# Performance work log

Hardware: AMD Instinct MI355X
Metric: run time of the kernel (lower is better)

Reference implementation:

```python
import jax, jax.numpy as jnp
import numpy as np

N = 50000      # nodes
E = 500000     # edges
IN = 256       # input feature dim
HID = 64       # hidden (per-head) dim, layer 1
H1 = 4         # heads, layer 1
NC = 64        # num_classes (layer 2 out, 1 head)
ED = 32        # edge_dim
T = 8          # num_etypes
SLOPE = 0.2    # leakyrelu negative slope


def setup_inputs() -> dict:
    key = jax.random.key(0)
    ks = jax.random.split(key, 20)
    p = lambda k, shape: (jax.random.normal(k, shape, jnp.float32) * 0.05)
    return {
        "h": jax.random.normal(ks[0], (N, IN), jnp.float32),
        "row": jax.random.randint(ks[1], (E,), 0, N, jnp.int32),   # src
        "col": jax.random.randint(ks[2], (E,), 0, N, jnp.int32),   # dst
        "etype": jax.random.randint(ks[3], (E,), 0, T, jnp.int32),
        # layer 1 (4 heads, no residual, elu activation)
        "edge_emb1": p(ks[4], (T, ED)),
        "W1": p(ks[5], (IN, HID * H1)),
        "Wr1": p(ks[6], (T, ED, ED * H1)),      # TypedLinear per-etype weight
        "a_l1": p(ks[7], (H1, HID)),
        "a_r1": p(ks[8], (H1, HID)),
        "a_e1": p(ks[9], (H1, ED)),
        # layer 2 (1 head, residual Linear, no activation)
        "edge_emb2": p(ks[10], (T, ED)),
        "W2": p(ks[11], (HID * H1, NC)),
        "Wr2": p(ks[12], (T, ED, ED)),
        "a_l2": p(ks[13], (1, NC)),
        "a_r2": p(ks[14], (1, NC)),
        "a_e2": p(ks[15], (1, ED)),
        "res_W2": p(ks[16], (HID * H1, NC)),
        "res_b2": p(ks[17], (NC,)),
    }


def _simple_hgn_conv(h, row, col, etype, edge_emb, W, Wr, a_l, a_r, a_e,
                     res_W, res_b, apply_act):
    """One SimpleHGNConv layer. h:[N,in], returns [N, out_dim*H] (D-major, H-minor
    layout, matching emb.permute(0,2,1).view in the torch code)."""
    H, D = a_l.shape            # num_heads, out_dim
    n = h.shape[0]
    emb = (h @ W).reshape(n, H, D)                     # [N,H,D]
    emb = jnp.where(jnp.isnan(emb), 0.0, emb)
    # TypedLinear: edge_emb[etype] @ Wr[etype]; only T distinct rows -> per-type GEMM
    ee = jnp.einsum('te,teo->to', edge_emb, Wr).reshape(T, H, ED)  # [T,H,ED]
    h_l = jnp.einsum('nhd,hd->nh', emb, a_l)[row]      # [E,H]
    h_r = jnp.einsum('nhd,hd->nh', emb, a_r)[col]      # [E,H]
    h_e = jnp.einsum('thd,hd->th', ee, a_e)[etype]     # [E,H]
    att = jax.nn.leaky_relu(h_l + h_r + h_e, SLOPE)    # [E,H]
    # edge_softmax: normalize over incoming edges of each destination node (col)
    seg_max = jax.ops.segment_max(att, col, num_segments=n)   # [N,H]
    att = jnp.exp(att - seg_max[col])
    seg_sum = jax.ops.segment_sum(att, col, num_segments=n)   # [N,H]
    alpha = att / seg_sum[col]                          # [E,H]
    # u_mul_e + sum aggregation
    msg = emb[row] * alpha[:, :, None]                  # [E,H,D]
    out = jax.ops.segment_sum(msg, col, num_segments=n) # [N,H,D]
    out = out.transpose(0, 2, 1).reshape(n, D * H)      # D-major layout
    if res_W is not None:
        out = out + h @ res_W + res_b
    if apply_act:
        out = jax.nn.elu(out)
    return out


def reference(h, row, col, etype,
              edge_emb1, W1, Wr1, a_l1, a_r1, a_e1,
              edge_emb2, W2, Wr2, a_l2, a_r2, a_e2, res_W2, res_b2):
    h1 = _simple_hgn_conv(h, row, col, etype, edge_emb1, W1, Wr1,
                          a_l1, a_r1, a_e1, None, None, True)
    h2 = _simple_hgn_conv(h1, row, col, etype, edge_emb2, W2, Wr2,
                          a_l2, a_r2, a_e2, res_W2, res_b2, False)
    # split by node type (first half type 'l', second half type 'v')
    return (h2[: N // 2], h2[N // 2 :])
```

## Files before the change

### kernel.cpp

```cpp
#include <hip/hip_runtime.h>
#include <hip/hip_bf16.h>

typedef __bf16 bf16x8 __attribute__((ext_vector_type(8)));
typedef float f32x4 __attribute__((ext_vector_type(4)));

#define IN_DIM 256
#define NT 8

__device__ __forceinline__ float b2f(unsigned short u) {
  union { unsigned int i; float f; } x; x.i = ((unsigned int)u) << 16; return x.f;
}
__device__ __forceinline__ float lo2f(unsigned int w) {
  union { unsigned int i; float f; } x; x.i = w << 16; return x.f;
}
__device__ __forceinline__ float hi2f(unsigned int w) {
  union { unsigned int i; float f; } x; x.i = w & 0xFFFF0000u; return x.f;
}
__device__ __forceinline__ unsigned short f2b(float f) {
  union { float f; unsigned int i; } u; u.f = f;
  unsigned int r = u.i + 0x7FFF + ((u.i >> 16) & 1);
  return (unsigned short)(r >> 16);
}
__device__ __forceinline__ float lrelu(float x) { return x >= 0.f ? x : 0.2f * x; }
__device__ __forceinline__ float ldf(const void* p, size_t i, int isf32) {
  return isf32 ? ((const float*)p)[i] : b2f(((const unsigned short*)p)[i]);
}

__global__ void detect_kernel(const unsigned int* __restrict__ hw, int* __restrict__ flag) {
  int tid = threadIdx.x;
  int bad = 0;
  for (int i = 0; i < 4; i++) {
    unsigned int w = hw[tid * 4 + i];
    unsigned int e = (w & 0x7FFFu) >> 7;
    if (e >= 0xC0u) bad++;
  }
#pragma unroll
  for (int off = 32; off; off >>= 1) bad += __shfl_xor(bad, off);
  if (tid == 0) *flag = (bad > 8) ? 1 : 0;
}

__global__ void prep_all_kernel(const void* __restrict__ W1, const void* __restrict__ W2,
                                const void* __restrict__ rW2,
                                const void* __restrict__ al1, const void* __restrict__ ar1,
                                const void* __restrict__ al2, const void* __restrict__ ar2,
                                const void* __restrict__ ee1, const void* __restrict__ Wr1,
                                const void* __restrict__ ae1,
                                const void* __restrict__ ee2, const void* __restrict__ Wr2,
                                const void* __restrict__ ae2,
                                unsigned short* __restrict__ W1t,
                                unsigned short* __restrict__ W2t,
                                float* __restrict__ a2l, float* __restrict__ a2r,
                                float* __restrict__ he1, float* __restrict__ he2,
                                float* __restrict__ alD, float* __restrict__ arD,
                                const int* __restrict__ dflag) {
  int isf32 = *dflag;
  int b = blockIdx.x, tid = threadIdx.x;
  if (b < 384) {
    int j = b, k = tid;
    if (j < 256) {
      int src = (j & 3) * 64 + (j >> 2);
      W1t[j * 256 + k] = f2b(ldf(W1, (size_t)k * 256 + src, isf32));
    } else {
      int o = j - 256;
      float v = (o < 64) ? ldf(W2, (size_t)k * 64 + o, isf32)
                         : ldf(rW2, (size_t)k * 64 + (o - 64), isf32);
      W2t[o * 256 + k] = f2b(v);
    }
  } else if (b < 448) {
    int k = (b - 384) * 4 + (tid >> 6), d = tid & 63;
    float w2 = ldf(W2, (size_t)k * 64 + d, isf32);
    float l2 = w2 * ldf(al2, d, isf32);
    float r2 = w2 * ldf(ar2, d, isf32);
#pragma unroll
    for (int off = 32; off; off >>= 1) { l2 += __shfl_xor(l2, off); r2 += __shfl_xor(r2, off); }
    if (d == 0) { a2l[k] = l2; a2r[k] = r2; }
  } else {
    int bid = b - 448;
    int t = tid >> 5, d = tid & 31;
    if (bid < 4) {
      int h = bid;
      float s = 0.f;
#pragma unroll
      for (int e = 0; e < 32; e++)
        s += ldf(ee1, t * 32 + e, isf32) * ldf(Wr1, (size_t)(t * 32 + e) * 128 + h * 32 + d, isf32);
      float v = s * ldf(ae1, h * 32 + d, isf32);
#pragma unroll
      for (int off = 16; off; off >>= 1) v += __shfl_xor(v, off);
      if (d == 0) he1[t * 4 + h] = v;
    } else if (bid == 4) {
      float s = 0.f;
#pragma unroll
      for (int e = 0; e < 32; e++)
        s += ldf(ee2, t * 32 + e, isf32) * ldf(Wr2, (size_t)(t * 32 + e) * 32 + d, isf32);
      float v = s * ldf(ae2, d, isf32);
#pragma unroll
      for (int off = 16; off; off >>= 1) v += __shfl_xor(v, off);
      if (d == 0) he2[t] = v;
    } else {
      int j = tid;
      alD[j] = ldf(al1, (j & 3) * 64 + (j >> 2), isf32);
      arD[j] = ldf(ar1, (j & 3) * 64 + (j >> 2), isf32);
    }
  }
}

__global__ __launch_bounds__(256, 2) void gemm1_fused(
    const void* __restrict__ A, int M,
    const unsigned short* __restrict__ Bt,
    unsigned short* __restrict__ emb1,
    const float* __restrict__ alD, const float* __restrict__ arD,
    float* __restrict__ hl1, float* __restrict__ hr1,
    const int* __restrict__ dflag) {
  __shared__ unsigned short As[64 * 64];
  __shared__ unsigned short Bs[256 * 64];
  __shared__ float lsum[4][64][4];
  __shared__ float rsum[4][64][4];
  int isf32 = *dflag;
  const int tid = threadIdx.x;
  const int m0 = blockIdx.x * 64;
  const int wv = tid >> 6, lane = tid & 63;
  const int q = lane >> 4, m = lane & 15;
  const int jp = wv * 64;
  f32x4 acc[4][4] = {};
  for (int kc = 0; kc < 256; kc += 64) {
    {
      int row = tid >> 2, qt = tid & 3;
      int gr = m0 + row;
      unsigned short tmp[16];
      if (gr < M) {
        if (isf32) {
          const float* ap = (const float*)A + (size_t)gr * 256 + kc + qt * 16;
          float4 v0 = *(const float4*)ap;
          float4 v1 = *(const float4*)(ap + 4);
          float4 v2 = *(const float4*)(ap + 8);
          float4 v3 = *(const float4*)(ap + 12);
          tmp[0]=f2b(v0.x); tmp[1]=f2b(v0.y); tmp[2]=f2b(v0.z); tmp[3]=f2b(v0.w);
          tmp[4]=f2b(v1.x); tmp[5]=f2b(v1.y); tmp[6]=f2b(v1.z); tmp[7]=f2b(v1.w);
          tmp[8]=f2b(v2.x); tmp[9]=f2b(v2.y); tmp[10]=f2b(v2.z); tmp[11]=f2b(v2.w);
          tmp[12]=f2b(v3.x); tmp[13]=f2b(v3.y); tmp[14]=f2b(v3.z); tmp[15]=f2b(v3.w);
        } else {
          const unsigned short* ap = (const unsigned short*)A + (size_t)gr * 256 + kc + qt * 16;
          *(int4*)tmp = *(const int4*)ap;
          *(int4*)(tmp + 8) = *(const int4*)(ap + 8);
        }
      } else {
        for (int x = 0; x < 16; x++) tmp[x] = 0;
      }
      int g0 = (qt * 2) ^ (row & 7);
      int g1 = (qt * 2 + 1) ^ (row & 7);
      *(int4*)(As + row * 64 + g0 * 8) = *(int4*)tmp;
      *(int4*)(As + row * 64 + g1 * 8) = *(int4*)(tmp + 8);
    }
    {
#pragma unroll
      for (int i = 0; i < 8; i++) {
        int id = tid + i * 256;
        int row = id >> 3, gg = id & 7;
        int4 v = *(const int4*)(Bt + (size_t)row * 256 + kc + gg * 8);
        int pg = gg ^ (row & 7);
        *(int4*)(Bs + row * 64 + pg * 8) = v;
      }
    }
    __syncthreads();
#pragma unroll
    for (int ks = 0; ks < 2; ks++) {
      int gk = ks * 4 + q;
      bf16x8 afr[4];
#pragma unroll
      for (int cm = 0; cm < 4; cm++) {
        int row = cm * 16 + m;
        afr[cm] = *(const bf16x8*)(As + row * 64 + (gk ^ (row & 7)) * 8);
      }
#pragma unroll
      for (int cj = 0; cj < 4; cj++) {
        int jr = jp + cj * 16 + m;
        bf16x8 b = *(const bf16x8*)(Bs + jr * 64 + (gk ^ (jr & 7)) * 8);
#pragma unroll
        for (int cm = 0; cm < 4; cm++)
          acc[cm][cj] = __builtin_amdgcn_mfma_f32_16x16x32_bf16(afr[cm], b, acc[cm][cj], 0, 0, 0);
      }
    }
    __syncthreads();
  }
  float al[4], ar[4];
#pragma unroll
  for (int cj = 0; cj < 4; cj++) {
    al[cj] = alD[jp + cj * 16 + m];
    ar[cj] = arD[jp + cj * 16 + m];
  }
#pragma unroll
  for (int cm = 0; cm < 4; cm++) {
#pragma unroll
    for (int r = 0; r < 4; r++) {
      int lrow = cm * 16 + q * 4 + r;
      int gm = m0 + lrow;
      float lp = 0.f, rp = 0.f;
#pragma unroll
      for (int cj = 0; cj < 4; cj++) {
        float v = acc[cm][cj][r];
        if (gm < M) emb1[(size_t)gm * 256 + jp + cj * 16 + m] = f2b(v);
        lp += v * al[cj]; rp += v * ar[cj];
      }
      lp += __shfl_xor(lp, 4); lp += __shfl_xor(lp, 8);
      rp += __shfl_xor(rp, 4); rp += __shfl_xor(rp, 8);
      if (m < 4) { lsum[wv][lrow][m] = lp; rsum[wv][lrow][m] = rp; }
    }
  }
  __syncthreads();
  {
    int row = tid >> 2, h = tid & 3;
    int gm = m0 + row;
    if (gm < M) {
      float l = lsum[0][row][h] + lsum[1][row][h] + lsum[2][row][h] + lsum[3][row][h];
      float r = rsum[0][row][h] + rsum[1][row][h] + rsum[2][row][h] + rsum[3][row][h];
      hl1[(size_t)gm * 4 + h] = l;
      hr1[(size_t)gm * 4 + h] = r;
    }
  }
}

__global__ __launch_bounds__(256, 2) void gemm2_fused(
    const unsigned short* __restrict__ A, int M,
    const unsigned short* __restrict__ Bt,
    unsigned short* __restrict__ emb2, unsigned short* __restrict__ res,
    const void* __restrict__ bias, const int* __restrict__ dflag) {
  __shared__ unsigned short As[64 * 64];
  __shared__ unsigned short Bs[128 * 64];
  int isf32 = *dflag;
  const int tid = threadIdx.x;
  const int m0 = blockIdx.x * 64;
  const int wv = tid >> 6, lane = tid & 63;
  const int q = lane >> 4, m = lane & 15;
  const int jp = (wv & 1) * 64;
  const int mh = (wv >> 1) * 32;
  f32x4 acc[2][4] = {};
  for (int kc = 0; kc < 256; kc += 64) {
    {
      int row = tid >> 2, qt = tid & 3;
      int gr = m0 + row;
      unsigned short tmp[16];
      if (gr < M) {
        const unsigned short* ap = A + (size_t)gr * 256 + kc + qt * 16;
        *(int4*)tmp = *(const int4*)ap;
        *(int4*)(tmp + 8) = *(const int4*)(ap + 8);
      } else {
        for (int x = 0; x < 16; x++) tmp[x] = 0;
      }
      int g0 = (qt * 2) ^ (row & 7);
      int g1 = (qt * 2 + 1) ^ (row & 7);
      *(int4*)(As + row * 64 + g0 * 8) = *(int4*)tmp;
      *(int4*)(As + row * 64 + g1 * 8) = *(int4*)(tmp + 8);
    }
    {
#pragma unroll
      for (int i = 0; i < 4; i++) {
        int id = tid + i * 256;
        int row = id >> 3, gg = id & 7;
        int4 v = *(const int4*)(Bt + (size_t)row * 256 + kc + gg * 8);
        int pg = gg ^ (row & 7);
        *(int4*)(Bs + row * 64 + pg * 8) = v;
      }
    }
    __syncthreads();
#pragma unroll
    for (int ks = 0; ks < 2; ks++) {
      int gk = ks * 4 + q;
      bf16x8 afr[2];
#pragma unroll
      for (int cm = 0; cm < 2; cm++) {
        int row = mh + cm * 16 + m;
        afr[cm] = *(const bf16x8*)(As + row * 64 + (gk ^ (row & 7)) * 8);
      }
#pragma unroll
      for (int cj = 0; cj < 4; cj++) {
        int jr = jp + cj * 16 + m;
        bf16x8 b = *(const bf16x8*)(Bs + jr * 64 + (gk ^ (jr & 7)) * 8);
#pragma unroll
        for (int cm = 0; cm < 2; cm++)
          acc[cm][cj] = __builtin_amdgcn_mfma_f32_16x16x32_bf16(afr[cm], b, acc[cm][cj], 0, 0, 0);
      }
    }
    __syncthreads();
  }
  float bv[4];
#pragma unroll
  for (int cj = 0; cj < 4; cj++)
    bv[cj] = (jp == 64) ? ldf(bias, cj * 16 + m, isf32) : 0.f;
#pragma unroll
  for (int cm = 0; cm < 2; cm++) {
#pragma unroll
    for (int r = 0; r < 4; r++) {
      int gm = m0 + mh + cm * 16 + q * 4 + r;
      if (gm < M) {
#pragma unroll
        for (int cj = 0; cj < 4; cj++) {
          float v = acc[cm][cj][r];
          int gj = cj * 16 + m;
          if (jp == 0) emb2[(size_t)gm * 64 + gj] = f2b(v);
          else res[(size_t)gm * 64 + gj] = f2b(v + bv[cj]);
        }
      }
    }
  }
}

__global__ void count_kernel(const int* __restrict__ col, int* __restrict__ cnt,
                             int E_, int N_) {
  int e = blockIdx.x * 256 + threadIdx.x;
  if (e >= E_) return;
  int c = col[e];
  if ((unsigned)c < (unsigned)N_) atomicAdd(&cnt[c], 1);
}

__global__ void scan1_kernel(const int* __restrict__ cnt, int* __restrict__ ptrb,
                             int* __restrict__ bsum, int n) {
  __shared__ int wsum[4];
  int tid = threadIdx.x, lane = tid & 63, wid = tid >> 6;
  int i = blockIdx.x * 256 + tid;
  int v = (i < n) ? cnt[i] : 0;
  int x = v;
#pragma unroll
  for (int off = 1; off < 64; off <<= 1) {
    int y = __shfl_up(x, off);
    if (lane >= off) x += y;
  }
  if (lane == 63) wsum[wid] = x;
  __syncthreads();
  int woff = 0;
#pragma unroll
  for (int k = 0; k < 4; k++) woff += (k < wid) ? wsum[k] : 0;
  if (i < n) ptrb[i] = x - v + woff;
  if (tid == 255) bsum[blockIdx.x] = woff + x;
}

__global__ void scan2_kernel(int* __restrict__ bsum, int* __restrict__ ptrb,
                             int nb, int n) {
  __shared__ int wsum[4];
  int tid = threadIdx.x, lane = tid & 63, wid = tid >> 6;
  int v = (tid < nb) ? bsum[tid] : 0;
  int x = v;
#pragma unroll
  for (int off = 1; off < 64; off <<= 1) {
    int y = __shfl_up(x, off);
    if (lane >= off) x += y;
  }
  if (lane == 63) wsum[wid] = x;
  __syncthreads();
  int woff = 0;
#pragma unroll
  for (int k = 0; k < 4; k++) woff += (k < wid) ? wsum[k] : 0;
  if (tid < nb) bsum[tid] = x - v + woff;
  if (tid == 255) ptrb[n] = woff + x;
}

__global__ void scan3_kernel(int* __restrict__ ptrb, const int* __restrict__ bsum, int n) {
  int i = blockIdx.x * 256 + threadIdx.x;
  if (i < n) ptrb[i] += bsum[blockIdx.x];
}

__global__ void fill_kernel(const int* __restrict__ col, const int* __restrict__ row,
                            const int* __restrict__ ety, const int* __restrict__ ptrb,
                            int* __restrict__ cnt, int* __restrict__ srcc, int E_, int N_) {
  int e = blockIdx.x * 256 + threadIdx.x;
  if (e >= E_) return;
  int c = col[e];
  if ((unsigned)c >= (unsigned)N_) return;
  int pos = atomicSub(&cnt[c], 1) - 1;
  long long slot = (long long)ptrb[c] + pos;
  if (slot >= 0 && slot < E_) {
    int sr = row[e], t = ety[e];
    srcc[slot] = ((unsigned)sr < (unsigned)N_ && (unsigned)t < (unsigned)NT)
                     ? (sr | (t << 20)) : -1;
  }
}

__global__ __launch_bounds__(256) void agg1_kernel(
    const int* __restrict__ ptrb, const int* __restrict__ srcc,
    const float* __restrict__ hl1, const float* __restrict__ hr1,
    const float* __restrict__ he1,
    const unsigned short* __restrict__ emb1, unsigned short* __restrict__ h1,
    const float* __restrict__ a2l, const float* __restrict__ a2r,
    float* __restrict__ hl2, float* __restrict__ hr2,
    int N_, int E_) {
  __shared__ float4 wds[4][64];
  __shared__ int sds[4][64];
  const int tid = threadIdx.x;
  const int wv = tid >> 6, lane = tid & 63;
  const int g = lane >> 4, ln = lane & 15;
  const int node = blockIdx.x * 16 + wv * 4 + g;
  const bool nv = node < N_;
  int p0 = 0, p1 = 0;
  if (nv) {
    p0 = ptrb[node]; p1 = ptrb[node + 1];
    p0 = max(0, min(p0, E_)); p1 = max(p0, min(p1, E_));
  }
  float4 hrv = {0.f, 0.f, 0.f, 0.f};
  if (nv) hrv = *(const float4*)(hr1 + 4 * (size_t)node);
  float s0 = 0.f, s1 = 0.f, s2 = 0.f, s3 = 0.f;
  float acc[16];
#pragma unroll
  for (int k = 0; k < 16; k++) acc[k] = 0.f;
  const unsigned short* erow = emb1 + ln * 16;
  for (int pb = p0;; pb += 16) {
    if (!__any(pb < p1)) break;
    int mc = (pb < p1) ? min(p1 - pb, 16) : 0;
    float4 w = {0.f, 0.f, 0.f, 0.f};
    int src = 0;
    if (ln < mc) {
      int spk = srcc[pb + ln];
      if (spk >= 0) {
        int sr = spk & 0xFFFFF, t = spk >> 20;
        float4 a = *(const float4*)(hl1 + 4 * (size_t)sr);
        float4 ge = *(const float4*)(he1 + 4 * (size_t)t);
        w.x = __expf(lrelu(a.x + hrv.x + ge.x));
        w.y = __expf(lrelu(a.y + hrv.y + ge.y));
        w.z = __expf(lrelu(a.z + hrv.z + ge.z));
        w.w = __expf(lrelu(a.w + hrv.w + ge.w));
        src = sr;
      }
    }
    s0 += w.x; s1 += w.y; s2 += w.z; s3 += w.w;
    wds[wv][lane] = w;
    sds[wv][lane] = src;
    for (int j = 0; j < mc; j += 2) {
      bool v1 = (j + 1) < mc;
      float4 u0 = wds[wv][g * 16 + j];
      int r0 = sds[wv][g * 16 + j];
      const unsigned short* e0 = erow + (size_t)r0 * 256;
      int4 ra = *(const int4*)e0;
      int4 rb = *(const int4*)(e0 + 8);
      float4 u1; int4 rc, rd;
      if (v1) {
        u1 = wds[wv][g * 16 + j + 1];
        int r1 = sds[wv][g * 16 + j + 1];
        const unsigned short* e1 = erow + (size_t)r1 * 256;
        rc = *(const int4*)e1;
        rd = *(const int4*)(e1 + 8);
      }
      acc[0]  += u0.x * lo2f(ra.x); acc[1]  += u0.y * hi2f(ra.x);
      acc[2]  += u0.z * lo2f(ra.y); acc[3]  += u0.w * hi2f(ra.y);
      acc[4]  += u0.x * lo2f(ra.z); acc[5]  += u0.y * hi2f(ra.z);
      acc[6]  += u0.z * lo2f(ra.w); acc[7]  += u0.w * hi2f(ra.w);
      acc[8]  += u0.x * lo2f(rb.x); acc[9]  += u0.y * hi2f(rb.x);
      acc[10] += u0.z * lo2f(rb.y); acc[11] += u0.w * hi2f(rb.y);
      acc[12] += u0.x * lo2f(rb.z); acc[13] += u0.y * hi2f(rb.z);
      acc[14] += u0.z * lo2f(rb.w); acc[15] += u0.w * hi2f(rb.w);
      if (v1) {
        acc[0]  += u1.x * lo2f(rc.x); acc[1]  += u1.y * hi2f(rc.x);
        acc[2]  += u1.z * lo2f(rc.y); acc[3]  += u1.w * hi2f(rc.y);
        acc[4]  += u1.x * lo2f(rc.z); acc[5]  += u1.y * hi2f(rc.z);
        acc[6]  += u1.z * lo2f(rc.w); acc[7]  += u1.w * hi2f(rc.w);
        acc[8]  += u1.x * lo2f(rd.x); acc[9]  += u1.y * hi2f(rd.x);
        acc[10] += u1.z * lo2f(rd.y); acc[11] += u1.w * hi2f(rd.y);
        acc[12] += u1.x * lo2f(rd.z); acc[13] += u1.y * hi2f(rd.z);
        acc[14] += u1.z * lo2f(rd.w); acc[15] += u1.w * hi2f(rd.w);
      }
    }
  }
#pragma unroll
  for (int off = 1; off < 16; off <<= 1) {
    s0 += __shfl_xor(s0, off); s1 += __shfl_xor(s1, off);
    s2 += __shfl_xor(s2, off); s3 += __shfl_xor(s3, off);
  }
  float invs[4];
  invs[0] = s0 > 0.f ? 1.f / s0 : 0.f;
  invs[1] = s1 > 0.f ? 1.f / s1 : 0.f;
  invs[2] = s2 > 0.f ? 1.f / s2 : 0.f;
  invs[3] = s3 > 0.f ? 1.f / s3 : 0.f;
  float alv[16], arv[16];
#pragma unroll
  for (int q2 = 0; q2 < 4; q2++) {
    float4 t1 = *(const float4*)(a2l + ln * 16 + q2 * 4);
    float4 t2 = *(const float4*)(a2r + ln * 16 + q2 * 4);
    alv[q2 * 4 + 0] = t1.x; alv[q2 * 4 + 1] = t1.y;
    alv[q2 * 4 + 2] = t1.z; alv[q2 * 4 + 3] = t1.w;
    arv[q2 * 4 + 0] = t2.x; arv[q2 * 4 + 1] = t2.y;
    arv[q2 * 4 + 2] = t2.z; arv[q2 * 4 + 3] = t2.w;
  }
  float lp = 0.f, rp = 0.f;
  unsigned int ow[8];
#pragma unroll
  for (int k = 0; k < 16; k++) {
    float r = acc[k] * invs[k & 3];
    r = r > 0.f ? r : __expf(r) - 1.f;
    unsigned int bb = f2b(r);
    if ((k & 1) == 0) ow[k >> 1] = bb; else ow[k >> 1] |= bb << 16;
    lp += r * alv[k];
    rp += r * arv[k];
  }
  if (nv) {
    int4 va; va.x = ow[0]; va.y = ow[1]; va.z = ow[2]; va.w = ow[3];
    int4 vb; vb.x = ow[4]; vb.y = ow[5]; vb.z = ow[6]; vb.w = ow[7];
    *(int4*)(h1 + (size_t)node * 256 + ln * 16) = va;
    *(int4*)(h1 + (size_t)node * 256 + ln * 16 + 8) = vb;
  }
#pragma unroll
  for (int off = 1; off < 16; off <<= 1) {
    lp += __shfl_xor(lp, off); rp += __shfl_xor(rp, off);
  }
  if (nv && ln == 0) { hl2[node] = lp; hr2[node] = rp; }
}

__global__ __launch_bounds__(256) void agg2_kernel(
    const int* __restrict__ ptrb, const int* __restrict__ srcc,
    const float* __restrict__ hl2, const float* __restrict__ hr2,
    const float* __restrict__ he2,
    const unsigned short* __restrict__ emb2, const unsigned short* __restrict__ res,
    void* __restrict__ out, int N_, int E_, const int* __restrict__ dflag) {
  __shared__ int2 wsd[4][64];
  const int isf32 = *dflag;
  const int tid = threadIdx.x;
  const int wv = tid >> 6, lane = tid & 63;
  const int g = lane >> 4, ln = lane & 15;
  const int node = blockIdx.x * 16 + wv * 4 + g;
  const bool nv = node < N_;
  int p0 = 0, p1 = 0;
  if (nv) {
    p0 = ptrb[node]; p1 = ptrb[node + 1];
    p0 = max(0, min(p0, E_)); p1 = max(p0, min(p1, E_));
  }
  float hrv = nv ? hr2[node] : 0.f;
  float s = 0.f;
  float acc[4] = {0.f, 0.f, 0.f, 0.f};
  const unsigned short* erow = emb2 + ln * 4;
  for (int pb = p0;; pb += 16) {
    if (!__any(pb < p1)) break;
    int mc = (pb < p1) ? min(p1 - pb, 16) : 0;
    float w = 0.f; int src = 0;
    if (ln < mc) {
      int spk = srcc[pb + ln];
      if (spk >= 0) {
        int sr = spk & 0xFFFFF, t = spk >> 20;
        w = __expf(lrelu(hl2[sr] + hrv + he2[t]));
        src = sr;
      }
    }
    s += w;
    int2 pk; pk.x = __float_as_int(w); pk.y = src;
    wsd[wv][lane] = pk;
    for (int j = 0; j < mc; j += 2) {
      bool v1 = (j + 1) < mc;
      int2 w0 = wsd[wv][g * 16 + j];
      float u0 = __int_as_float(w0.x);
      int2 ra = *(const int2*)(erow + (size_t)w0.y * 64);
      float u1 = 0.f; int2 rc;
      if (v1) {
        int2 w1 = wsd[wv][g * 16 + j + 1];
        u1 = __int_as_float(w1.x);
        rc = *(const int2*)(erow + (size_t)w1.y * 64);
      }
      acc[0] += u0 * lo2f(ra.x); acc[1] += u0 * hi2f(ra.x);
      acc[2] += u0 * lo2f(ra.y); acc[3] += u0 * hi2f(ra.y);
      if (v1) {
        acc[0] += u1 * lo2f(rc.x); acc[1] += u1 * hi2f(rc.x);
        acc[2] += u1 * lo2f(rc.y); acc[3] += u1 * hi2f(rc.y);
      }
    }
  }
#pragma unroll
  for (int off = 1; off < 16; off <<= 1) s += __shfl_xor(s, off);
  float inv = s > 0.f ? 1.f / s : 0.f;
  if (nv) {
    ushort4 rv = *(const ushort4*)(res + (size_t)node * 64 + ln * 4);
    float o0 = acc[0] * inv + b2f(rv.x);
    float o1 = acc[1] * inv + b2f(rv.y);
    float o2 = acc[2] * inv + b2f(rv.z);
    float o3 = acc[3] * inv + b2f(rv.w);
    size_t oi = (size_t)node * 64 + ln * 4;
    if (isf32) {
      float4 ov = {o0, o1, o2, o3};
      *(float4*)((float*)out + oi) = ov;
    } else {
      ushort4 ov; ov.x = f2b(o0); ov.y = f2b(o1); ov.z = f2b(o2); ov.w = f2b(o3);
      *(ushort4*)((unsigned short*)out + oi) = ov;
    }
  }
}

extern "C" void kernel_launch(void* const* d_in, const int* in_sizes, int n_in,
                              void* d_out, int out_size, void* d_ws, size_t ws_size,
                              hipStream_t stream) {
  const int N = in_sizes[0] / IN_DIM;
  const int E = in_sizes[1];

  const void* h   = d_in[0];
  const int* row  = (const int*)d_in[1];
  const int* col  = (const int*)d_in[2];
  const int* ety  = (const int*)d_in[3];
  const void* ee1 = d_in[4];
  const void* W1  = d_in[5];
  const void* Wr1 = d_in[6];
  const void* al1 = d_in[7];
  const void* ar1 = d_in[8];
  const void* ae1 = d_in[9];
  const void* ee2 = d_in[10];
  const void* W2  = d_in[11];
  const void* Wr2 = d_in[12];
  const void* al2 = d_in[13];
  const void* ar2 = d_in[14];
  const void* ae2 = d_in[15];
  const void* rW2 = d_in[16];
  const void* rb2 = d_in[17];

  char* p = (char*)d_ws;
  auto take = [&](size_t b) { char* q = p; p += (b + 255) & ~(size_t)255; return q; };
  unsigned short* h1   = (unsigned short*)take((size_t)N * 256 * 2);
  unsigned short* emb1 = (unsigned short*)take((size_t)N * 256 * 2);
  int* srcc = (int*)take((size_t)E * 4);
  int* ptrb = (int*)take((size_t)(N + 1) * 4);
  int* cnt  = (int*)take((size_t)N * 4);
  int* bsum = (int*)take(1024);
  float* hl1 = (float*)take((size_t)N * 4 * 4);
  float* hr1 = (float*)take((size_t)N * 4 * 4);
  float* hl2 = (float*)take((size_t)N * 4);
  float* hr2 = (float*)take((size_t)N * 4);
  unsigned short* W1t = (unsigned short*)take(256 * 256 * 2);
  unsigned short* W2t = (unsigned short*)take(128 * 256 * 2);
  float* a2l = (float*)take(256 * 4);
  float* a2r = (float*)take(256 * 4);
  float* alD = (float*)take(256 * 4);
  float* arD = (float*)take(256 * 4);
  float* he1 = (float*)take(NT * 4 * 4);
  float* he2 = (float*)take(NT * 4);
  int* dflag = (int*)take(256);
  unsigned short* emb2 = emb1;
  unsigned short* res  = emb1 + (size_t)N * 64;

  const size_t need = (size_t)(p - (char*)d_ws);
  if (need > ws_size) {
    hipMemsetAsync(d_out, 0, (size_t)out_size * 2, stream);
    return;
  }

  const int EB = (E + 255) / 256;
  const int MB = (N + 63) / 64;
  const int SB = (N + 255) / 256;
  const int AB = (N + 15) / 16;

  detect_kernel<<<1, 64, 0, stream>>>((const unsigned int*)h, dflag);
  hipMemsetAsync(cnt, 0, (size_t)N * 4, stream);
  prep_all_kernel<<<454, 256, 0, stream>>>(W1, W2, rW2, al1, ar1, al2, ar2,
                                           ee1, Wr1, ae1, ee2, Wr2, ae2,
                                           W1t, W2t, a2l, a2r, he1, he2, alD, arD, dflag);

  count_kernel<<<EB, 256, 0, stream>>>(col, cnt, E, N);
  scan1_kernel<<<SB, 256, 0, stream>>>(cnt, ptrb, bsum, N);
  scan2_kernel<<<1, 256, 0, stream>>>(bsum, ptrb, SB, N);
  scan3_kernel<<<SB, 256, 0, stream>>>(ptrb, bsum, N);
  fill_kernel<<<EB, 256, 0, stream>>>(col, row, ety, ptrb, cnt, srcc, E, N);

  gemm1_fused<<<MB, 256, 0, stream>>>(h, N, W1t, emb1, alD, arD, hl1, hr1, dflag);
  agg1_kernel<<<AB, 256, 0, stream>>>(
      ptrb, srcc, hl1, hr1, he1, emb1, h1, a2l, a2r, hl2, hr2, N, E);

  gemm2_fused<<<MB, 256, 0, stream>>>(h1, N, W2t, emb2, res, rb2, dflag);
  agg2_kernel<<<AB, 256, 0, stream>>>(
      ptrb, srcc, hl2, hr2, he2, emb2, res, d_out, N, E, dflag);
}
```

Baseline: 273.6 us.

## Fold detect and count into prep kernel, drop scan3, prefetch agg2 gathers

```diff
diff --git a/kernel.cpp b/kernel.cpp
--- a/kernel.cpp
+++ b/kernel.cpp
@@ -24,19 +24,6 @@
 __device__ __forceinline__ float lrelu(float x) { return x >= 0.f ? x : 0.2f * x; }
 __device__ __forceinline__ float ldf(const void* p, size_t i, int isf32) {
   return isf32 ? ((const float*)p)[i] : b2f(((const unsigned short*)p)[i]);
-}
-
-__global__ void detect_kernel(const unsigned int* __restrict__ hw, int* __restrict__ flag) {
-  int tid = threadIdx.x;
-  int bad = 0;
-  for (int i = 0; i < 4; i++) {
-    unsigned int w = hw[tid * 4 + i];
-    unsigned int e = (w & 0x7FFFu) >> 7;
-    if (e >= 0xC0u) bad++;
-  }
-#pragma unroll
-  for (int off = 32; off; off >>= 1) bad += __shfl_xor(bad, off);
-  if (tid == 0) *flag = (bad > 8) ? 1 : 0;
 }
 
 __global__ void prep_all_kernel(const void* __restrict__ W1, const void* __restrict__ W2,
@@ -52,9 +39,35 @@
                                 float* __restrict__ a2l, float* __restrict__ a2r,
                                 float* __restrict__ he1, float* __restrict__ he2,
                                 float* __restrict__ alD, float* __restrict__ arD,
-                                const int* __restrict__ dflag) {
-  int isf32 = *dflag;
+                                const unsigned int* __restrict__ hw,
+                                const int* __restrict__ col, int* __restrict__ cnt,
+                                int E_, int N_, int* __restrict__ dflag) {
   int b = blockIdx.x, tid = threadIdx.x;
+  if (b >= 454) {
+    int e = (b - 454) * 256 + tid;
+    if (e < E_) {
+      int c = col[e];
+      if ((unsigned)c < (unsigned)N_) atomicAdd(&cnt[c], 1);
+    }
+    return;
+  }
+  __shared__ int sflag;
+  {
+    int bad = 0;
+    if (tid < 64) {
+      for (int i = 0; i < 4; i++) {
+        unsigned int w = hw[tid * 4 + i];
+        unsigned int ex = (w & 0x7FFFu) >> 7;
+        if (ex >= 0xC0u) bad++;
+      }
+#pragma unroll
+      for (int off = 32; off; off >>= 1) bad += __shfl_xor(bad, off);
+      if (tid == 0) sflag = (bad > 8) ? 1 : 0;
+    }
+    __syncthreads();
+  }
+  const int isf32 = sflag;
+  if (b == 0 && tid == 0) *dflag = isf32;
   if (b < 384) {
     int j = b, k = tid;
     if (j < 256) {
@@ -304,14 +317,6 @@
   }
 }
 
-__global__ void count_kernel(const int* __restrict__ col, int* __restrict__ cnt,
-                             int E_, int N_) {
-  int e = blockIdx.x * 256 + threadIdx.x;
-  if (e >= E_) return;
-  int c = col[e];
-  if ((unsigned)c < (unsigned)N_) atomicAdd(&cnt[c], 1);
-}
-
 __global__ void scan1_kernel(const int* __restrict__ cnt, int* __restrict__ ptrb,
                              int* __restrict__ bsum, int n) {
   __shared__ int wsum[4];
@@ -353,20 +358,16 @@
   if (tid == 255) ptrb[n] = woff + x;
 }
 
-__global__ void scan3_kernel(int* __restrict__ ptrb, const int* __restrict__ bsum, int n) {
-  int i = blockIdx.x * 256 + threadIdx.x;
-  if (i < n) ptrb[i] += bsum[blockIdx.x];
-}
-
 __global__ void fill_kernel(const int* __restrict__ col, const int* __restrict__ row,
                             const int* __restrict__ ety, const int* __restrict__ ptrb,
+                            const int* __restrict__ bsum,
                             int* __restrict__ cnt, int* __restrict__ srcc, int E_, int N_) {
   int e = blockIdx.x * 256 + threadIdx.x;
   if (e >= E_) return;
   int c = col[e];
   if ((unsigned)c >= (unsigned)N_) return;
   int pos = atomicSub(&cnt[c], 1) - 1;
-  long long slot = (long long)ptrb[c] + pos;
+  long long slot = (long long)(ptrb[c] + bsum[c >> 8]) + pos;
   if (slot >= 0 && slot < E_) {
     int sr = row[e], t = ety[e];
     srcc[slot] = ((unsigned)sr < (unsigned)N_ && (unsigned)t < (unsigned)NT)
@@ -375,7 +376,8 @@
 }
 
 __global__ __launch_bounds__(256) void agg1_kernel(
-    const int* __restrict__ ptrb, const int* __restrict__ srcc,
+    const int* __restrict__ ptrb, const int* __restrict__ bsumv,
+    const int* __restrict__ srcc,
     const float* __restrict__ hl1, const float* __restrict__ hr1,
     const float* __restrict__ he1,
     const unsigned short* __restrict__ emb1, unsigned short* __restrict__ h1,
@@ -391,7 +393,8 @@
   const bool nv = node < N_;
   int p0 = 0, p1 = 0;
   if (nv) {
-    p0 = ptrb[node]; p1 = ptrb[node + 1];
+    p0 = ptrb[node] + bsumv[node >> 8];
+    p1 = (node + 1 < N_) ? (ptrb[node + 1] + bsumv[(node + 1) >> 8]) : ptrb[N_];
     p0 = max(0, min(p0, E_)); p1 = max(p0, min(p1, E_));
   }
   float4 hrv = {0.f, 0.f, 0.f, 0.f};
@@ -502,12 +505,13 @@
 }
 
 __global__ __launch_bounds__(256) void agg2_kernel(
-    const int* __restrict__ ptrb, const int* __restrict__ srcc,
+    const int* __restrict__ ptrb, const int* __restrict__ bsumv,
+    const int* __restrict__ srcc,
     const float* __restrict__ hl2, const float* __restrict__ hr2,
     const float* __restrict__ he2,
     const unsigned short* __restrict__ emb2, const unsigned short* __restrict__ res,
     void* __restrict__ out, int N_, int E_, const int* __restrict__ dflag) {
-  __shared__ int2 wsd[4][64];
+  __shared__ int2 wsd[4][4][17];
   const int isf32 = *dflag;
   const int tid = threadIdx.x;
   const int wv = tid >> 6, lane = tid & 63;
@@ -516,7 +520,8 @@
   const bool nv = node < N_;
   int p0 = 0, p1 = 0;
   if (nv) {
-    p0 = ptrb[node]; p1 = ptrb[node + 1];
+    p0 = ptrb[node] + bsumv[node >> 8];
+    p1 = (node + 1 < N_) ? (ptrb[node + 1] + bsumv[(node + 1) >> 8]) : ptrb[N_];
     p0 = max(0, min(p0, E_)); p1 = max(p0, min(p1, E_));
   }
   float hrv = nv ? hr2[node] : 0.f;
@@ -537,24 +542,23 @@
     }
     s += w;
     int2 pk; pk.x = __float_as_int(w); pk.y = src;
-    wsd[wv][lane] = pk;
+    wsd[wv][g][ln] = pk;
+    int2 w0 = {0, 0}, w1 = {0, 0}; int2 pa = {0, 0}, pc = {0, 0};
+    if (0 < mc) { w0 = wsd[wv][g][0]; pa = *(const int2*)(erow + (size_t)w0.y * 64); }
+    if (1 < mc) { w1 = wsd[wv][g][1]; pc = *(const int2*)(erow + (size_t)w1.y * 64); }
     for (int j = 0; j < mc; j += 2) {
-      bool v1 = (j + 1) < mc;
-      int2 w0 = wsd[wv][g * 16 + j];
+      int2 nw0 = {0, 0}, nw1 = {0, 0}, na = {0, 0}, nc = {0, 0};
+      if (j + 2 < mc) { nw0 = wsd[wv][g][j + 2]; na = *(const int2*)(erow + (size_t)nw0.y * 64); }
+      if (j + 3 < mc) { nw1 = wsd[wv][g][j + 3]; nc = *(const int2*)(erow + (size_t)nw1.y * 64); }
       float u0 = __int_as_float(w0.x);
-      int2 ra = *(const int2*)(erow + (size_t)w0.y * 64);
-      float u1 = 0.f; int2 rc;
-      if (v1) {
-        int2 w1 = wsd[wv][g * 16 + j + 1];
-        u1 = __int_as_float(w1.x);
-        rc = *(const int2*)(erow + (size_t)w1.y * 64);
-      }
-      acc[0] += u0 * lo2f(ra.x); acc[1] += u0 * hi2f(ra.x);
-      acc[2] += u0 * lo2f(ra.y); acc[3] += u0 * hi2f(ra.y);
-      if (v1) {
-        acc[0] += u1 * lo2f(rc.x); acc[1] += u1 * hi2f(rc.x);
-        acc[2] += u1 * lo2f(rc.y); acc[3] += u1 * hi2f(rc.y);
-      }
+      acc[0] += u0 * lo2f(pa.x); acc[1] += u0 * hi2f(pa.x);
+      acc[2] += u0 * lo2f(pa.y); acc[3] += u0 * hi2f(pa.y);
+      if (j + 1 < mc) {
+        float u1 = __int_as_float(w1.x);
+        acc[0] += u1 * lo2f(pc.x); acc[1] += u1 * hi2f(pc.x);
+        acc[2] += u1 * lo2f(pc.y); acc[3] += u1 * hi2f(pc.y);
+      }
+      w0 = nw0; w1 = nw1; pa = na; pc = nc;
     }
   }
 #pragma unroll
@@ -637,23 +641,21 @@
   const int SB = (N + 255) / 256;
   const int AB = (N + 15) / 16;
 
-  detect_kernel<<<1, 64, 0, stream>>>((const unsigned int*)h, dflag);
   hipMemsetAsync(cnt, 0, (size_t)N * 4, stream);
-  prep_all_kernel<<<454, 256, 0, stream>>>(W1, W2, rW2, al1, ar1, al2, ar2,
-                                           ee1, Wr1, ae1, ee2, Wr2, ae2,
-                                           W1t, W2t, a2l, a2r, he1, he2, alD, arD, dflag);
-
-  count_kernel<<<EB, 256, 0, stream>>>(col, cnt, E, N);
+  prep_all_kernel<<<454 + EB, 256, 0, stream>>>(
+      W1, W2, rW2, al1, ar1, al2, ar2, ee1, Wr1, ae1, ee2, Wr2, ae2,
+      W1t, W2t, a2l, a2r, he1, he2, alD, arD,
+      (const unsigned int*)h, col, cnt, E, N, dflag);
+
   scan1_kernel<<<SB, 256, 0, stream>>>(cnt, ptrb, bsum, N);
   scan2_kernel<<<1, 256, 0, stream>>>(bsum, ptrb, SB, N);
-  scan3_kernel<<<SB, 256, 0, stream>>>(ptrb, bsum, N);
-  fill_kernel<<<EB, 256, 0, stream>>>(col, row, ety, ptrb, cnt, srcc, E, N);
+  fill_kernel<<<EB, 256, 0, stream>>>(col, row, ety, ptrb, bsum, cnt, srcc, E, N);
 
   gemm1_fused<<<MB, 256, 0, stream>>>(h, N, W1t, emb1, alD, arD, hl1, hr1, dflag);
   agg1_kernel<<<AB, 256, 0, stream>>>(
-      ptrb, srcc, hl1, hr1, he1, emb1, h1, a2l, a2r, hl2, hr2, N, E);
+      ptrb, bsum, srcc, hl1, hr1, he1, emb1, h1, a2l, a2r, hl2, hr2, N, E);
 
   gemm2_fused<<<MB, 256, 0, stream>>>(h1, N, W2t, emb2, res, rb2, dflag);
   agg2_kernel<<<AB, 256, 0, stream>>>(
-      ptrb, srcc, hl2, hr2, he2, emb2, res, d_out, N, E, dflag);
-}
+      ptrb, bsum, srcc, hl2, hr2, he2, emb2, res, d_out, N, E, dflag);
+}
```

After: 267.2 us. 2.3% less time.
